# Optimization experiments

Hardware: AMD Instinct MI355X
Metric: run time of the kernel (lower is better)

## Reference

```python
import jax, jax.numpy as jnp
import numpy as np

NUM_CLASSES = 80
S = 7            # grid_size
NB = 2           # num_boxes per cell
LAMBDA_COORD = 5.0
LAMBDA_NOOBJ = 0.5
N_BOX = 20       # padded boxes per image


def setup_inputs() -> dict:
    key = jax.random.key(0)
    k1, k2, k3, k4 = jax.random.split(key, 4)
    B = 4096
    predictions = jax.random.uniform(k1, (B, S, S, NB, 5 + NUM_CLASSES), dtype=jnp.float32)
    # build valid normalized xyxy boxes: centers in [0.1,0.9], half-sizes in [0.01,0.085]
    centers = jax.random.uniform(k2, (B, N_BOX, 2), dtype=jnp.float32) * 0.8 + 0.1
    half = jax.random.uniform(k3, (B, N_BOX, 2), dtype=jnp.float32) * 0.075 + 0.01
    targets_boxes = jnp.concatenate([centers - half, centers + half], axis=-1)
    targets_labels = jax.random.randint(k4, (B, N_BOX), 0, NUM_CLASSES)
    return {"predictions": predictions, "targets_boxes": targets_boxes, "targets_labels": targets_labels}


def encode_targets(boxes, labels):
    # boxes: [B,N,4] xyxy normalized; labels: [B,N] int
    B, N, _ = boxes.shape
    x = (boxes[..., 0] + boxes[..., 2]) * 0.5
    y = (boxes[..., 1] + boxes[..., 3]) * 0.5
    w = boxes[..., 2] - boxes[..., 0]
    h = boxes[..., 3] - boxes[..., 1]
    j = jnp.clip(jnp.floor(x * S).astype(jnp.int32), 0, S - 1)
    i = jnp.clip(jnp.floor(y * S).astype(jnp.int32), 0, S - 1)
    x_cell = x * S - j
    y_cell = y * S - i
    onehot = jax.nn.one_hot(labels, NUM_CLASSES, dtype=boxes.dtype)
    feats = jnp.concatenate([x_cell[..., None], y_cell[..., None], w[..., None], h[..., None],
                             jnp.ones_like(x_cell)[..., None], onehot], axis=-1)  # [B,N,5+C]
    bidx = jnp.arange(B, dtype=jnp.int32)[:, None]
    flat = ((bidx * S + i) * S + j).ravel()                       # [B*N] cell ids
    order = jnp.broadcast_to(jnp.arange(N, dtype=jnp.int32), (B, N)).ravel()
    winner = jnp.full((B * S * S,), N, dtype=jnp.int32).at[flat].min(order)
    cell_b = jnp.arange(B * S * S, dtype=jnp.int32) // (S * S)
    sel = jnp.minimum(winner, N - 1)
    grid = feats[cell_b, sel]
    grid = jnp.where((winner < N)[:, None], grid, jnp.zeros_like(grid))
    return grid.reshape(B, S, S, 5 + NUM_CLASSES)


def iou_xywh(a, b):
    ax1 = a[..., 0] - a[..., 2] * 0.5; ay1 = a[..., 1] - a[..., 3] * 0.5
    ax2 = a[..., 0] + a[..., 2] * 0.5; ay2 = a[..., 1] + a[..., 3] * 0.5
    bx1 = b[..., 0] - b[..., 2] * 0.5; by1 = b[..., 1] - b[..., 3] * 0.5
    bx2 = b[..., 0] + b[..., 2] * 0.5; by2 = b[..., 1] + b[..., 3] * 0.5
    iw = jnp.clip(jnp.minimum(ax2, bx2) - jnp.maximum(ax1, bx1), 0.0)
    ih = jnp.clip(jnp.minimum(ay2, by2) - jnp.maximum(ay1, by1), 0.0)
    inter = iw * ih
    union = (ax2 - ax1) * (ay2 - ay1) + (bx2 - bx1) * (by2 - by1) - inter
    return inter / (union + 1e-6)


def yolo_loss(predictions, targets_boxes, targets_labels):
    B = predictions.shape[0]
    tg = encode_targets(targets_boxes, targets_labels)   # [B,S,S,5+C]
    txy, twh = tg[..., :2], tg[..., 2:4]
    tconf, tcls = tg[..., 4:5], tg[..., 5:]
    obj = (tconf[..., 0] > 0).astype(predictions.dtype)   # [B,S,S]
    # responsible box = argmax IoU per cell, masked by obj
    pred_boxes = predictions[..., 0:4]                     # [B,S,S,NB,4]
    tgt_boxes = jnp.concatenate([txy, twh], axis=-1)[:, :, :, None, :]
    ious = iou_xywh(pred_boxes, jnp.broadcast_to(tgt_boxes, pred_boxes.shape))  # [B,S,S,NB]
    best = jnp.argmax(ious, axis=-1)
    resp = jax.nn.one_hot(best, NB, dtype=predictions.dtype) * obj[..., None]   # [B,S,S,NB]
    pxy = predictions[..., 0:2]; pwh = predictions[..., 2:4]
    pconf = predictions[..., 4:5]; pcls = predictions[..., 5:]
    om = obj[..., None, None]        # [B,S,S,1,1]
    rm = resp[..., None]             # [B,S,S,NB,1]
    loss_xy = LAMBDA_COORD * jnp.sum(om * rm * (pxy - txy[:, :, :, None, :]) ** 2) / B
    loss_wh = LAMBDA_COORD * jnp.sum(om * rm * (jnp.sqrt(jnp.clip(pwh, 1e-6)) - jnp.sqrt(jnp.clip(twh[:, :, :, None, :], 1e-6))) ** 2) / B
    loss_conf_obj = jnp.sum(om * rm * (pconf - tconf[:, :, :, None, :]) ** 2) / B
    loss_conf_noobj = LAMBDA_NOOBJ * jnp.sum((1.0 - obj)[..., None, None] * pconf ** 2) / B
    pred_cls_resp = jnp.sum(pcls * rm, axis=3)             # [B,S,S,C]
    loss_cls = jnp.sum(obj[..., None] * (pred_cls_resp - tcls) ** 2) / B
    return loss_xy + loss_wh + loss_conf_obj + loss_conf_noobj + loss_cls


def reference(predictions, targets_boxes, targets_labels):
    return yolo_loss(predictions, targets_boxes, targets_labels)
```

## Files before the change

kernel.cpp:

```cpp
#include <hip/hip_runtime.h>

#define S 7
#define NB 2
#define NC 80
#define NBOX 20
#define CELLS 49
#define CH 85
#define PAIR 170
#define PER_B 8330
#define NIMG 4096
#define NBOXSLOT (NIMG*CELLS*NB)
#define N4TOT (NIMG*PER_B/4)
#define PREP_IMGS 4
#define PREP_BLOCKS (NIMG/PREP_IMGS)
#define STREAM_BLOCKS 1960
#define STREAM_ITERS 17
#define L_COORD 5.0f
#define L_NOOBJ 0.5f

typedef float vfloat4 __attribute__((ext_vector_type(4)));

__device__ __forceinline__ void block_reduce_store(float acc, float* dst)
{
    __shared__ float s_wsum[4];
    int tid = threadIdx.x;
    #pragma unroll
    for (int off = 32; off > 0; off >>= 1) acc += __shfl_down(acc, off, 64);
    int lane = tid & 63, wv = tid >> 6;
    if (lane == 0) s_wsum[wv] = acc;
    __syncthreads();
    if (tid == 0) *dst = s_wsum[0] + s_wsum[1] + s_wsum[2] + s_wsum[3];
}

__global__ __launch_bounds__(256) void prep_kernel(
    const float* __restrict__ pred,
    const float* __restrict__ boxes,
    const int*   __restrict__ labels,
    float*       __restrict__ wb,
    float*       __restrict__ partial)
{
    __shared__ int   s_winner[PREP_IMGS * CELLS];
    __shared__ float s_cx[PREP_IMGS * NBOX], s_cy[PREP_IMGS * NBOX];
    __shared__ float s_bw[PREP_IMGS * NBOX], s_bh[PREP_IMGS * NBOX];
    __shared__ int   s_lab[PREP_IMGS * NBOX];

    const int b0  = blockIdx.x * PREP_IMGS;
    const int tid = threadIdx.x;

    if (tid < PREP_IMGS * CELLS) s_winner[tid] = NBOX;
    __syncthreads();

    if (tid < PREP_IMGS * NBOX) {
        int img = tid / NBOX, bxi = tid - img * NBOX;
        const float* bx = boxes + ((size_t)(b0 + img) * NBOX + bxi) * 4;
        float x1 = bx[0], y1 = bx[1], x2 = bx[2], y2 = bx[3];
        float x = (x1 + x2) * 0.5f, y = (y1 + y2) * 0.5f;
        s_cx[tid] = x; s_cy[tid] = y;
        s_bw[tid] = x2 - x1; s_bh[tid] = y2 - y1;
        s_lab[tid] = labels[(size_t)(b0 + img) * NBOX + bxi];
        int j = (int)floorf(x * (float)S); j = min(max(j, 0), S - 1);
        int i = (int)floorf(y * (float)S); i = min(max(i, 0), S - 1);
        atomicMin(&s_winner[img * CELLS + i * S + j], bxi);
    }
    __syncthreads();

    float acc = 0.0f;
    if (tid < PREP_IMGS * CELLS) {
        int img  = tid / CELLS;
        int cell = tid - img * CELLS;
        int w    = s_winner[tid];
        size_t slot = ((size_t)(b0 + img) * CELLS + cell) * 2;
        const float* p = pred + ((size_t)(b0 + img) * CELLS + cell) * PAIR;
        float w0 = 0.f, w1 = 0.f;
        if (w < NBOX) {
            int i = cell / S, j = cell - (cell / S) * S;
            int bi = img * NBOX + w;
            float x = s_cx[bi], y = s_cy[bi];
            float tx = x * (float)S - (float)j;
            float ty = y * (float)S - (float)i;
            float tw = s_bw[bi], th = s_bh[bi];

            float bx1 = tx - tw * 0.5f, by1 = ty - th * 0.5f;
            float bx2 = tx + tw * 0.5f, by2 = ty + th * 0.5f;
            float barea = (bx2 - bx1) * (by2 - by1);
            float iou[2], px[2], py[2], pw[2], ph[2];
            #pragma unroll
            for (int nb = 0; nb < NB; nb++) {
                px[nb] = p[nb * CH + 0]; py[nb] = p[nb * CH + 1];
                pw[nb] = p[nb * CH + 2]; ph[nb] = p[nb * CH + 3];
                float ax1 = px[nb] - pw[nb] * 0.5f, ay1 = py[nb] - ph[nb] * 0.5f;
                float ax2 = px[nb] + pw[nb] * 0.5f, ay2 = py[nb] + ph[nb] * 0.5f;
                float iw = fmaxf(fminf(ax2, bx2) - fmaxf(ax1, bx1), 0.0f);
                float ih = fmaxf(fminf(ay2, by2) - fmaxf(ay1, by1), 0.0f);
                float inter = iw * ih;
                float uni = (ax2 - ax1) * (ay2 - ay1) + barea - inter;
                iou[nb] = inter / (uni + 1e-6f);
            }
            int resp = (iou[1] > iou[0]) ? 1 : 0;
            w0 = (resp == 0) ? 1.f : 0.f;
            w1 = 1.f - w0;

            float pc = p[resp * CH + 4];
            float pl = p[resp * CH + 5 + s_lab[bi]];
            float dx = px[resp] - tx, dy = py[resp] - ty;
            float dw = sqrtf(fmaxf(pw[resp], 1e-6f)) - sqrtf(fmaxf(tw, 1e-6f));
            float dh = sqrtf(fmaxf(ph[resp], 1e-6f)) - sqrtf(fmaxf(th, 1e-6f));
            acc = L_COORD * (dx * dx + dy * dy + dw * dw + dh * dh)
                + (1.0f - 2.0f * pc)
                + (1.0f - 2.0f * pl)
                - (px[resp] * px[resp] + py[resp] * py[resp]
                 + pw[resp] * pw[resp] + ph[resp] * ph[resp]);
        } else {
            float c0 = p[4], c1 = p[CH + 4];
            acc = L_NOOBJ * (c0 * c0 + c1 * c1);
        }
        wb[slot]     = w0;
        wb[slot + 1] = w1;
    }
    __syncthreads();
    block_reduce_store(acc, &partial[blockIdx.x]);
}

__global__ __launch_bounds__(256) void stream_kernel(
    const vfloat4* __restrict__ p4,
    const float*   __restrict__ wb,
    float*         __restrict__ partial)
{
    const int tid  = threadIdx.x;
    const int base = blockIdx.x * (STREAM_ITERS * 256);

    float acc = 0.0f;
    #pragma unroll
    for (int k = 0; k < STREAM_ITERS; ++k) {
        int e = base + k * 256 + tid;
        vfloat4 v = __builtin_nontemporal_load(&p4[e]);
        unsigned ff = 4u * (unsigned)e;
        unsigned bi = ff / 85u;
        int r85 = (int)(ff - bi * 85u);
        int thr = 85 - r85;
        float wa = wb[bi];
        float wn = wb[bi + 1];
        float w1 = (1 < thr) ? wa : wn;
        float w2 = (2 < thr) ? wa : wn;
        float w3 = (3 < thr) ? wa : wn;
        acc += wa * (v.x * v.x);
        acc += w1 * (v.y * v.y);
        acc += w2 * (v.z * v.z);
        acc += w3 * (v.w * v.w);
    }
    block_reduce_store(acc, &partial[blockIdx.x]);
}

__global__ __launch_bounds__(256) void reduce_kernel(
    const float* __restrict__ partial, int n,
    float* __restrict__ out, float inv_B)
{
    const int tid = threadIdx.x;
    float acc = 0.0f;
    for (int i = tid; i < n; i += 256) acc += partial[i];
    __shared__ float s_wsum[4];
    #pragma unroll
    for (int off = 32; off > 0; off >>= 1) acc += __shfl_down(acc, off, 64);
    int lane = tid & 63, wv = tid >> 6;
    if (lane == 0) s_wsum[wv] = acc;
    __syncthreads();
    if (tid == 0) out[0] = (s_wsum[0] + s_wsum[1] + s_wsum[2] + s_wsum[3]) * inv_B;
}

extern "C" void kernel_launch(void* const* d_in, const int* in_sizes, int n_in,
                              void* d_out, int out_size, void* d_ws, size_t ws_size,
                              hipStream_t stream) {
    const float* pred   = (const float*)d_in[0];
    const float* boxes  = (const float*)d_in[1];
    const int*   labels = (const int*)d_in[2];

    float* wb          = (float*)d_ws;
    float* prep_part   = wb + NBOXSLOT + 16;
    float* stream_part = prep_part + PREP_BLOCKS;

    prep_kernel<<<PREP_BLOCKS, 256, 0, stream>>>(pred, boxes, labels, wb, prep_part);
    stream_kernel<<<STREAM_BLOCKS, 256, 0, stream>>>((const vfloat4*)pred, wb, stream_part);
    reduce_kernel<<<1, 256, 0, stream>>>(prep_part, PREP_BLOCKS + STREAM_BLOCKS,
                                         (float*)d_out, 1.0f / (float)NIMG);
}
```

Baseline: 204.6 us.

## Use one thread per cell in prep, atomic final reduction, drop nontemporal loads

The prep kernel now maps one thread per grid cell across all 256 lanes. Each thread scans the image's 20 boxes to find the first box that claims its cell, replacing the shared-memory atomicMin scheme that left many threads idle. The separate reduce kernel is removed: each block atomically adds its scaled partial into the output, which is zeroed with a memset. The stream kernel's nontemporal loads become plain loads, which may let the second pass hit cache lines the prep kernel already touched. Float atomic accumulation makes the result order-nondeterministic, and the memset adds a small extra operation.

```diff
diff --git a/kernel.cpp b/kernel.cpp
--- a/kernel.cpp
+++ b/kernel.cpp
@@ -9,18 +9,19 @@
 #define PAIR 170
 #define PER_B 8330
 #define NIMG 4096
+#define NCELL_TOT (NIMG*CELLS)
 #define NBOXSLOT (NIMG*CELLS*NB)
 #define N4TOT (NIMG*PER_B/4)
-#define PREP_IMGS 4
-#define PREP_BLOCKS (NIMG/PREP_IMGS)
+#define PREP_BLOCKS (NCELL_TOT/256)
 #define STREAM_BLOCKS 1960
 #define STREAM_ITERS 17
 #define L_COORD 5.0f
 #define L_NOOBJ 0.5f
+#define INV_B (1.0f/4096.0f)
 
 typedef float vfloat4 __attribute__((ext_vector_type(4)));
 
-__device__ __forceinline__ void block_reduce_store(float acc, float* dst)
+__device__ __forceinline__ void block_reduce_atomic(float acc, float* out)
 {
     __shared__ float s_wsum[4];
     int tid = threadIdx.x;
@@ -29,102 +30,88 @@
     int lane = tid & 63, wv = tid >> 6;
     if (lane == 0) s_wsum[wv] = acc;
     __syncthreads();
-    if (tid == 0) *dst = s_wsum[0] + s_wsum[1] + s_wsum[2] + s_wsum[3];
+    if (tid == 0)
+        atomicAdd(out, (s_wsum[0] + s_wsum[1] + s_wsum[2] + s_wsum[3]) * INV_B);
 }
 
 __global__ __launch_bounds__(256) void prep_kernel(
     const float* __restrict__ pred,
     const float* __restrict__ boxes,
     const int*   __restrict__ labels,
-    float*       __restrict__ wb,
-    float*       __restrict__ partial)
+    float2*      __restrict__ wb2,
+    float*       __restrict__ out)
 {
-    __shared__ int   s_winner[PREP_IMGS * CELLS];
-    __shared__ float s_cx[PREP_IMGS * NBOX], s_cy[PREP_IMGS * NBOX];
-    __shared__ float s_bw[PREP_IMGS * NBOX], s_bh[PREP_IMGS * NBOX];
-    __shared__ int   s_lab[PREP_IMGS * NBOX];
+    const int tid   = threadIdx.x;
+    const int gcell = blockIdx.x * 256 + tid;
+    const unsigned img = (unsigned)gcell / (unsigned)CELLS;
+    const int cell  = gcell - (int)img * CELLS;
 
-    const int b0  = blockIdx.x * PREP_IMGS;
-    const int tid = threadIdx.x;
+    const float* bx = boxes + (size_t)img * NBOX * 4;
+    int winner = NBOX;
+    float wx = 0.f, wy = 0.f, wwd = 0.f, wht = 0.f;
+    #pragma unroll 4
+    for (int b = NBOX - 1; b >= 0; --b) {
+        float x1 = bx[4*b], y1 = bx[4*b+1], x2 = bx[4*b+2], y2 = bx[4*b+3];
+        float x = (x1 + x2) * 0.5f, y = (y1 + y2) * 0.5f;
+        int j = min(max((int)floorf(x * (float)S), 0), S - 1);
+        int i = min(max((int)floorf(y * (float)S), 0), S - 1);
+        if (i * S + j == cell) {
+            winner = b; wx = x; wy = y; wwd = x2 - x1; wht = y2 - y1;
+        }
+    }
 
-    if (tid < PREP_IMGS * CELLS) s_winner[tid] = NBOX;
-    __syncthreads();
+    const float* p = pred + (size_t)gcell * PAIR;
+    float acc;
+    float2 w;
+    if (winner < NBOX) {
+        int i = cell / S, j = cell - (cell / S) * S;
+        float tx = wx * (float)S - (float)j;
+        float ty = wy * (float)S - (float)i;
+        float tw = wwd, th = wht;
 
-    if (tid < PREP_IMGS * NBOX) {
-        int img = tid / NBOX, bxi = tid - img * NBOX;
-        const float* bx = boxes + ((size_t)(b0 + img) * NBOX + bxi) * 4;
-        float x1 = bx[0], y1 = bx[1], x2 = bx[2], y2 = bx[3];
-        float x = (x1 + x2) * 0.5f, y = (y1 + y2) * 0.5f;
-        s_cx[tid] = x; s_cy[tid] = y;
-        s_bw[tid] = x2 - x1; s_bh[tid] = y2 - y1;
-        s_lab[tid] = labels[(size_t)(b0 + img) * NBOX + bxi];
-        int j = (int)floorf(x * (float)S); j = min(max(j, 0), S - 1);
-        int i = (int)floorf(y * (float)S); i = min(max(i, 0), S - 1);
-        atomicMin(&s_winner[img * CELLS + i * S + j], bxi);
+        float bx1 = tx - tw * 0.5f, by1 = ty - th * 0.5f;
+        float bx2 = tx + tw * 0.5f, by2 = ty + th * 0.5f;
+        float barea = (bx2 - bx1) * (by2 - by1);
+        float iou[2], px[2], py[2], pw[2], ph[2];
+        #pragma unroll
+        for (int nb = 0; nb < NB; nb++) {
+            px[nb] = p[nb * CH + 0]; py[nb] = p[nb * CH + 1];
+            pw[nb] = p[nb * CH + 2]; ph[nb] = p[nb * CH + 3];
+            float ax1 = px[nb] - pw[nb] * 0.5f, ay1 = py[nb] - ph[nb] * 0.5f;
+            float ax2 = px[nb] + pw[nb] * 0.5f, ay2 = py[nb] + ph[nb] * 0.5f;
+            float iw = fmaxf(fminf(ax2, bx2) - fmaxf(ax1, bx1), 0.0f);
+            float ih = fmaxf(fminf(ay2, by2) - fmaxf(ay1, by1), 0.0f);
+            float inter = iw * ih;
+            float uni = (ax2 - ax1) * (ay2 - ay1) + barea - inter;
+            iou[nb] = inter / (uni + 1e-6f);
+        }
+        int resp = (iou[1] > iou[0]) ? 1 : 0;
+        w = (resp == 0) ? make_float2(1.f, 0.f) : make_float2(0.f, 1.f);
+
+        int lab = labels[img * NBOX + winner];
+        float pc = p[resp * CH + 4];
+        float pl = p[resp * CH + 5 + lab];
+        float dx = px[resp] - tx, dy = py[resp] - ty;
+        float dw = sqrtf(fmaxf(pw[resp], 1e-6f)) - sqrtf(fmaxf(tw, 1e-6f));
+        float dh = sqrtf(fmaxf(ph[resp], 1e-6f)) - sqrtf(fmaxf(th, 1e-6f));
+        acc = L_COORD * (dx * dx + dy * dy + dw * dw + dh * dh)
+            + (1.0f - 2.0f * pc)
+            + (1.0f - 2.0f * pl)
+            - (px[resp] * px[resp] + py[resp] * py[resp]
+             + pw[resp] * pw[resp] + ph[resp] * ph[resp]);
+    } else {
+        float c0 = p[4], c1 = p[CH + 4];
+        acc = L_NOOBJ * (c0 * c0 + c1 * c1);
+        w = make_float2(0.f, 0.f);
     }
-    __syncthreads();
-
-    float acc = 0.0f;
-    if (tid < PREP_IMGS * CELLS) {
-        int img  = tid / CELLS;
-        int cell = tid - img * CELLS;
-        int w    = s_winner[tid];
-        size_t slot = ((size_t)(b0 + img) * CELLS + cell) * 2;
-        const float* p = pred + ((size_t)(b0 + img) * CELLS + cell) * PAIR;
-        float w0 = 0.f, w1 = 0.f;
-        if (w < NBOX) {
-            int i = cell / S, j = cell - (cell / S) * S;
-            int bi = img * NBOX + w;
-            float x = s_cx[bi], y = s_cy[bi];
-            float tx = x * (float)S - (float)j;
-            float ty = y * (float)S - (float)i;
-            float tw = s_bw[bi], th = s_bh[bi];
-
-            float bx1 = tx - tw * 0.5f, by1 = ty - th * 0.5f;
-            float bx2 = tx + tw * 0.5f, by2 = ty + th * 0.5f;
-            float barea = (bx2 - bx1) * (by2 - by1);
-            float iou[2], px[2], py[2], pw[2], ph[2];
-            #pragma unroll
-            for (int nb = 0; nb < NB; nb++) {
-                px[nb] = p[nb * CH + 0]; py[nb] = p[nb * CH + 1];
-                pw[nb] = p[nb * CH + 2]; ph[nb] = p[nb * CH + 3];
-                float ax1 = px[nb] - pw[nb] * 0.5f, ay1 = py[nb] - ph[nb] * 0.5f;
-                float ax2 = px[nb] + pw[nb] * 0.5f, ay2 = py[nb] + ph[nb] * 0.5f;
-                float iw = fmaxf(fminf(ax2, bx2) - fmaxf(ax1, bx1), 0.0f);
-                float ih = fmaxf(fminf(ay2, by2) - fmaxf(ay1, by1), 0.0f);
-                float inter = iw * ih;
-                float uni = (ax2 - ax1) * (ay2 - ay1) + barea - inter;
-                iou[nb] = inter / (uni + 1e-6f);
-            }
-            int resp = (iou[1] > iou[0]) ? 1 : 0;
-            w0 = (resp == 0) ? 1.f : 0.f;
-            w1 = 1.f - w0;
-
-            float pc = p[resp * CH + 4];
-            float pl = p[resp * CH + 5 + s_lab[bi]];
-            float dx = px[resp] - tx, dy = py[resp] - ty;
-            float dw = sqrtf(fmaxf(pw[resp], 1e-6f)) - sqrtf(fmaxf(tw, 1e-6f));
-            float dh = sqrtf(fmaxf(ph[resp], 1e-6f)) - sqrtf(fmaxf(th, 1e-6f));
-            acc = L_COORD * (dx * dx + dy * dy + dw * dw + dh * dh)
-                + (1.0f - 2.0f * pc)
-                + (1.0f - 2.0f * pl)
-                - (px[resp] * px[resp] + py[resp] * py[resp]
-                 + pw[resp] * pw[resp] + ph[resp] * ph[resp]);
-        } else {
-            float c0 = p[4], c1 = p[CH + 4];
-            acc = L_NOOBJ * (c0 * c0 + c1 * c1);
-        }
-        wb[slot]     = w0;
-        wb[slot + 1] = w1;
-    }
-    __syncthreads();
-    block_reduce_store(acc, &partial[blockIdx.x]);
+    wb2[gcell] = w;
+    block_reduce_atomic(acc, out);
 }
 
 __global__ __launch_bounds__(256) void stream_kernel(
     const vfloat4* __restrict__ p4,
     const float*   __restrict__ wb,
-    float*         __restrict__ partial)
+    float*         __restrict__ out)
 {
     const int tid  = threadIdx.x;
     const int base = blockIdx.x * (STREAM_ITERS * 256);
@@ -133,7 +120,7 @@
     #pragma unroll
     for (int k = 0; k < STREAM_ITERS; ++k) {
         int e = base + k * 256 + tid;
-        vfloat4 v = __builtin_nontemporal_load(&p4[e]);
+        vfloat4 v = p4[e];
         unsigned ff = 4u * (unsigned)e;
         unsigned bi = ff / 85u;
         int r85 = (int)(ff - bi * 85u);
@@ -148,23 +135,7 @@
         acc += w2 * (v.z * v.z);
         acc += w3 * (v.w * v.w);
     }
-    block_reduce_store(acc, &partial[blockIdx.x]);
-}
-
-__global__ __launch_bounds__(256) void reduce_kernel(
-    const float* __restrict__ partial, int n,
-    float* __restrict__ out, float inv_B)
-{
-    const int tid = threadIdx.x;
-    float acc = 0.0f;
-    for (int i = tid; i < n; i += 256) acc += partial[i];
-    __shared__ float s_wsum[4];
-    #pragma unroll
-    for (int off = 32; off > 0; off >>= 1) acc += __shfl_down(acc, off, 64);
-    int lane = tid & 63, wv = tid >> 6;
-    if (lane == 0) s_wsum[wv] = acc;
-    __syncthreads();
-    if (tid == 0) out[0] = (s_wsum[0] + s_wsum[1] + s_wsum[2] + s_wsum[3]) * inv_B;
+    block_reduce_atomic(acc, out);
 }
 
 extern "C" void kernel_launch(void* const* d_in, const int* in_sizes, int n_in,
@@ -173,13 +144,12 @@
     const float* pred   = (const float*)d_in[0];
     const float* boxes  = (const float*)d_in[1];
     const int*   labels = (const int*)d_in[2];
+    float* out = (float*)d_out;
 
-    float* wb          = (float*)d_ws;
-    float* prep_part   = wb + NBOXSLOT + 16;
-    float* stream_part = prep_part + PREP_BLOCKS;
+    float* wb = (float*)d_ws;
 
-    prep_kernel<<<PREP_BLOCKS, 256, 0, stream>>>(pred, boxes, labels, wb, prep_part);
-    stream_kernel<<<STREAM_BLOCKS, 256, 0, stream>>>((const vfloat4*)pred, wb, stream_part);
-    reduce_kernel<<<1, 256, 0, stream>>>(prep_part, PREP_BLOCKS + STREAM_BLOCKS,
-                                         (float*)d_out, 1.0f / (float)NIMG);
+    hipMemsetAsync(d_out, 0, sizeof(float) * out_size, stream);
+    prep_kernel<<<PREP_BLOCKS, 256, 0, stream>>>(pred, boxes, labels,
+                                                 (float2*)wb, out);
+    stream_kernel<<<STREAM_BLOCKS, 256, 0, stream>>>((const vfloat4*)pred, wb, out);
 }
```

Measured after the change: 219.0 us. 1.07x slower.
